# Optimization experiments

Measured on AMD Instinct MI355X. Metric: run time of the kernel, lower is better.

Reference implementation:

```python
import jax, jax.numpy as jnp
import numpy as np

BN_EPS = 1e-5

def setup_inputs() -> dict:
    key = jax.random.key(0)
    ks = jax.random.split(key, 6)
    B, C, H, W, K = 16, 512, 64, 64, 32
    return {
        "x": jax.random.normal(ks[0], (B, C, H, W), dtype=jnp.float32),
        "conv_w": jax.random.normal(ks[1], (C, C), dtype=jnp.float32) * (1.0 / np.sqrt(C)),
        "conv_b": jax.random.normal(ks[2], (C,), dtype=jnp.float32) * 0.01,
        "codewords": jax.random.normal(ks[3], (K, C), dtype=jnp.float32) * (1.0 / np.sqrt(C)),
        "scale": jax.random.uniform(ks[4], (K,), dtype=jnp.float32, minval=-1.0, maxval=0.0),
        "bn_gamma": jnp.ones((K,), jnp.float32),
        "bn_beta": jnp.zeros((K,), jnp.float32),
        "bn_mean": jnp.zeros((K,), jnp.float32),
        "bn_var": jnp.ones((K,), jnp.float32),
        "fc_w": jax.random.normal(ks[5], (C, C), dtype=jnp.float32) * (1.0 / np.sqrt(C)),
        "fc_b": jnp.zeros((C,), jnp.float32),
    }

def reference(x, conv_w, conv_b, codewords, scale, bn_gamma, bn_beta, bn_mean, bn_var, fc_w, fc_b):
    B, C, H, W = x.shape
    N = H * W
    # 1x1 conv projection: (B,C,H,W) x (O,C) -> (B,O,H,W)
    proj = jnp.einsum('bchw,oc->bohw', x, conv_w) + conv_b[None, :, None, None]
    z = proj.reshape(B, C, N).transpose(0, 2, 1)  # (B, N, C)
    # scaled L2 distances without materializing (B,N,K,C):
    # ||z - cw||^2 = ||z||^2 - 2 z.cw + ||cw||^2
    z_sq = jnp.sum(z * z, axis=-1)                     # (B, N)
    cw_sq = jnp.sum(codewords * codewords, axis=-1)    # (K,)
    cross = jnp.einsum('bnc,kc->bnk', z, codewords)    # (B, N, K)
    dist = scale[None, None, :] * (z_sq[:, :, None] - 2.0 * cross + cw_sq[None, None, :])
    assign = jax.nn.softmax(dist, axis=2)              # (B, N, K)
    # aggregate: sum_n a[b,n,k] * (z[b,n,c] - cw[k,c])
    enc = jnp.einsum('bnk,bnc->bkc', assign, z) - jnp.sum(assign, axis=1)[:, :, None] * codewords[None]  # (B, K, C)
    # BatchNorm1d(num_codes) in eval mode normalizes the K (feature) axis, then ReLU
    inv_std = jax.lax.rsqrt(bn_var + BN_EPS)
    enc_bn = (enc - bn_mean[None, :, None]) * (inv_std * bn_gamma)[None, :, None] + bn_beta[None, :, None]
    encoding_feat = jnp.mean(jax.nn.relu(enc_bn), axis=1)  # (B, C)
    # sigmoid channel gate + residual fuse
    gamma = jax.nn.sigmoid(encoding_feat @ fc_w.T + fc_b)  # (B, C)
    y = gamma[:, :, None, None]
    output = jax.nn.relu(x + x * y)
    return (encoding_feat, output)
```

## Files before the change

kernel.cpp:

```cpp
#include <hip/hip_runtime.h>
#include <hip/hip_bf16.h>
#include <stdint.h>

#define DEV static __device__ __forceinline__

typedef __attribute__((ext_vector_type(8))) short bf16x8;
typedef __attribute__((ext_vector_type(4))) float f32x4;

DEV void async_ld16(const void* g, void* l) {
  __builtin_amdgcn_global_load_lds(
      (const __attribute__((address_space(1))) void*)g,
      (__attribute__((address_space(3))) void*)l, 16, 0, 0);
}

DEV unsigned short f2bf(float f) {
  union { __hip_bfloat16 h; unsigned short u; } c;
  c.h = __float2bfloat16(f);
  return c.u;
}

#define Bb 16
#define Cc 512
#define Nn 4096
#define Kk 32
#define NSPLIT 32

__global__ void k_castw(const float* __restrict__ a, __hip_bfloat16* __restrict__ o) {
  int i = blockIdx.x * 256 + threadIdx.x;
  o[i] = __float2bfloat16(a[i]);
}

__global__ void k_cw(const float* __restrict__ cw, __hip_bfloat16* __restrict__ cwb,
                     float* __restrict__ cwsq) {
  int k = blockIdx.x, lane = threadIdx.x;
  float s = 0.f;
#pragma unroll
  for (int j = 0; j < 8; ++j) {
    float v = cw[k * Cc + lane * 8 + j];
    cwb[k * Cc + lane * 8 + j] = __float2bfloat16(v);
    s += v * v;
  }
  for (int off = 32; off; off >>= 1) s += __shfl_down(s, off);
  if (lane == 0) cwsq[k] = s;
}

__global__ __launch_bounds__(256, 4) void k_gemm_z(const float* __restrict__ X,
                                                   const __hip_bfloat16* __restrict__ Bw,
                                                   const float* __restrict__ bias,
                                                   __hip_bfloat16* __restrict__ Z) {
  constexpr int AE = 128 * 32;
  constexpr int BE = 128 * 32;
  __shared__ __align__(16) unsigned short As[2 * AE];
  __shared__ __align__(16) __hip_bfloat16 Bs[2 * BE];
  const int b = blockIdx.y;
  const int n0 = (blockIdx.x & 31) * 128;
  const int c0 = (blockIdx.x >> 5) * 128;
  const int tid = threadIdx.x;
  const int lane = tid & 63, wid = tid >> 6;
  const int wr = (wid >> 1) * 64, wc = (wid & 1) * 64;
  const int cg = tid & 7;
  const int ng = tid >> 3;
  const float* Xb = X + (size_t)b * Cc * Nn + n0 + ng * 4;
  const __hip_bfloat16* Bbp = Bw + (size_t)c0 * Cc;
  f32x4 acc[4][4] = {};
  float4 av[4];
#pragma unroll
  for (int i = 0; i < 4; ++i)
    av[i] = *(const float4*)&Xb[(size_t)(cg * 4 + i) * Nn];
  int cur = 0;
  for (int kt = 0; kt < 16; ++kt) {
    unsigned short* Aw = As + cur * AE;
#pragma unroll
    for (int j = 0; j < 4; ++j) {
      int row = ng * 4 + j;
      int q = (cg >> 1) ^ ((row >> 1) & 3);
      ushort4 w;
      w.x = f2bf(av[0][j]);
      w.y = f2bf(av[1][j]);
      w.z = f2bf(av[2][j]);
      w.w = f2bf(av[3][j]);
      *(ushort4*)&Aw[row * 32 + q * 8 + (cg & 1) * 4] = w;
    }
    char* Bwr = (char*)(Bs + cur * BE);
#pragma unroll
    for (int j = 0; j < 2; ++j) {
      int li = tid + j * 256;
      int row = li >> 2;
      int kc = ((li & 3) ^ ((li >> 3) & 3)) * 8;
      async_ld16(Bbp + (size_t)row * Cc + kt * 32 + kc, Bwr + li * 16);
    }
    __syncthreads();
    if (kt < 15) {
#pragma unroll
      for (int i = 0; i < 4; ++i)
        av[i] = *(const float4*)&Xb[(size_t)((kt + 1) * 32 + cg * 4 + i) * Nn];
    }
    const unsigned short* Ar = As + cur * AE;
    const __hip_bfloat16* Br = Bs + cur * BE;
    bf16x8 af[4], bfv[4];
#pragma unroll
    for (int m = 0; m < 4; ++m) {
      int row = wr + m * 16 + (lane & 15);
      int q = (lane >> 4) ^ ((row >> 1) & 3);
      af[m] = *(const bf16x8*)&Ar[row * 32 + q * 8];
    }
#pragma unroll
    for (int nf = 0; nf < 4; ++nf) {
      int row = wc + nf * 16 + (lane & 15);
      int q = (lane >> 4) ^ ((row >> 1) & 3);
      bfv[nf] = *(const bf16x8*)&Br[row * 32 + q * 8];
    }
#pragma unroll
    for (int m = 0; m < 4; ++m)
#pragma unroll
      for (int nf = 0; nf < 4; ++nf)
        acc[m][nf] = __builtin_amdgcn_mfma_f32_16x16x32_bf16(af[m], bfv[nf], acc[m][nf], 0, 0, 0);
    cur ^= 1;
  }
  __hip_bfloat16* Zb = Z + ((size_t)b * Nn + n0) * Cc + c0;
#pragma unroll
  for (int nf = 0; nf < 4; ++nf) {
    int col = wc + nf * 16 + (lane & 15);
    float bv = bias[c0 + col];
#pragma unroll
    for (int m = 0; m < 4; ++m) {
#pragma unroll
      for (int r = 0; r < 4; ++r) {
        int row = wr + m * 16 + (lane >> 4) * 4 + r;
        Zb[(size_t)row * Cc + col] = __float2bfloat16(acc[m][nf][r] + bv);
      }
    }
  }
}

__global__ __launch_bounds__(256) void k_cross(const __hip_bfloat16* __restrict__ Z,
                                               const __hip_bfloat16* __restrict__ CW,
                                               const float* __restrict__ scale,
                                               const float* __restrict__ cwsq,
                                               float* __restrict__ assign,
                                               float* __restrict__ asum) {
  __shared__ __align__(16) __hip_bfloat16 As[128 * 32];
  __shared__ __align__(16) __hip_bfloat16 Bs[32 * 32];
  __shared__ float s_zsq[128];
  __shared__ float s_asum[Kk];
  int b = blockIdx.y;
  int n0 = blockIdx.x * 128;
  int tid = threadIdx.x, lane = tid & 63, wid = tid >> 6;
  if (tid < Kk) s_asum[tid] = 0.f;
  const __hip_bfloat16* Ab = Z + ((size_t)b * Nn + n0) * Cc;
  f32x4 acc[2][2] = {};
  float sq = 0.f;
  for (int kt = 0; kt < 16; ++kt) {
    int k0 = kt * 32;
    __syncthreads();
#pragma unroll
    for (int j = 0; j < 2; ++j) {
      int li = tid + j * 256;
      int row = li >> 2;
      int kc = ((li & 3) ^ ((li >> 3) & 3)) * 8;
      async_ld16(Ab + (size_t)row * Cc + k0 + kc, (char*)As + li * 16);
    }
    if (tid < 128) {
      int row = tid >> 2;
      int kc = ((tid & 3) ^ ((tid >> 3) & 3)) * 8;
      async_ld16(CW + (size_t)row * Cc + k0 + kc, (char*)Bs + tid * 16);
    }
    __syncthreads();
    {
      int row = tid >> 1, h = tid & 1;
      int rsw = (row >> 1) & 3;
#pragma unroll
      for (int c8 = 0; c8 < 2; ++c8) {
        union { bf16x8 v; __hip_bfloat16 e[8]; } t;
        t.v = *(const bf16x8*)&As[row * 32 + (((2 * h + c8) ^ rsw) * 8)];
#pragma unroll
        for (int i = 0; i < 8; ++i) {
          float v = __bfloat162float(t.e[i]);
          sq += v * v;
        }
      }
    }
    bf16x8 af[2], bfv[2];
#pragma unroll
    for (int m = 0; m < 2; ++m) {
      int row = wid * 32 + m * 16 + (lane & 15);
      int q = (lane >> 4) ^ ((row >> 1) & 3);
      af[m] = *(const bf16x8*)&As[row * 32 + q * 8];
    }
#pragma unroll
    for (int nf = 0; nf < 2; ++nf) {
      int row = nf * 16 + (lane & 15);
      int q = (lane >> 4) ^ ((row >> 1) & 3);
      bfv[nf] = *(const bf16x8*)&Bs[row * 32 + q * 8];
    }
#pragma unroll
    for (int m = 0; m < 2; ++m)
#pragma unroll
      for (int nf = 0; nf < 2; ++nf)
        acc[m][nf] = __builtin_amdgcn_mfma_f32_16x16x32_bf16(af[m], bfv[nf], acc[m][nf], 0, 0, 0);
  }
  sq += __shfl_xor(sq, 1);
  if ((tid & 1) == 0) s_zsq[tid >> 1] = sq;
  __syncthreads();
  float sc[2], cq[2];
#pragma unroll
  for (int nf = 0; nf < 2; ++nf) {
    sc[nf] = scale[nf * 16 + (lane & 15)];
    cq[nf] = cwsq[nf * 16 + (lane & 15)];
  }
  float asump0 = 0.f, asump1 = 0.f;
#pragma unroll
  for (int m = 0; m < 2; ++m) {
#pragma unroll
    for (int r = 0; r < 4; ++r) {
      int row = wid * 32 + m * 16 + (lane >> 4) * 4 + r;
      float zq = s_zsq[row];
      float v0 = sc[0] * (zq - 2.f * acc[m][0][r] + cq[0]);
      float v1 = sc[1] * (zq - 2.f * acc[m][1][r] + cq[1]);
      float mx = fmaxf(v0, v1);
#pragma unroll
      for (int off = 1; off < 16; off <<= 1) mx = fmaxf(mx, __shfl_xor(mx, off));
      float e0 = __expf(v0 - mx), e1 = __expf(v1 - mx);
      float s = e0 + e1;
#pragma unroll
      for (int off = 1; off < 16; off <<= 1) s += __shfl_xor(s, off);
      float inv = 1.f / s;
      float a0 = e0 * inv, a1 = e1 * inv;
      acc[m][0][r] = a0;
      acc[m][1][r] = a1;
      asump0 += a0;
      asump1 += a1;
    }
  }
  asump0 += __shfl_xor(asump0, 16); asump0 += __shfl_xor(asump0, 32);
  asump1 += __shfl_xor(asump1, 16); asump1 += __shfl_xor(asump1, 32);
  if (lane < 16) {
    atomicAdd(&s_asum[lane], asump0);
    atomicAdd(&s_asum[16 + lane], asump1);
  }
  float* Cb = assign + ((size_t)b * Nn + n0) * Kk;
#pragma unroll
  for (int m = 0; m < 2; ++m)
#pragma unroll
    for (int nf = 0; nf < 2; ++nf) {
      int col = nf * 16 + (lane & 15);
#pragma unroll
      for (int r = 0; r < 4; ++r) {
        int row = wid * 32 + m * 16 + (lane >> 4) * 4 + r;
        Cb[(size_t)row * Kk + col] = acc[m][nf][r];
      }
    }
  __syncthreads();
  if (tid < Kk) atomicAdd(&asum[b * Kk + tid], s_asum[tid]);
}

__global__ __launch_bounds__(256) void k_enc_part(const float* __restrict__ assign,
                                                  const __hip_bfloat16* __restrict__ Z,
                                                  float* __restrict__ part) {
  __shared__ float sa[128][Kk];
  int b = blockIdx.z;
  int s = blockIdx.y;
  int c = blockIdx.x * 256 + threadIdx.x;
  int tid = threadIdx.x;
  int n0 = s * 128;
  const float* ap = assign + ((size_t)b * Nn + n0) * Kk;
  for (int i = tid; i < 128 * Kk; i += 256) sa[i >> 5][i & 31] = ap[i];
  __syncthreads();
  float acc[Kk];
#pragma unroll
  for (int k = 0; k < Kk; ++k) acc[k] = 0.f;
  const __hip_bfloat16* zp = Z + ((size_t)b * Nn + n0) * Cc + c;
  for (int n = 0; n < 128; ++n) {
    float zv = __bfloat162float(zp[(size_t)n * Cc]);
    const float4* sp = (const float4*)&sa[n][0];
#pragma unroll
    for (int q = 0; q < 8; ++q) {
      float4 a4 = sp[q];
      acc[4 * q + 0] = fmaf(a4.x, zv, acc[4 * q + 0]);
      acc[4 * q + 1] = fmaf(a4.y, zv, acc[4 * q + 1]);
      acc[4 * q + 2] = fmaf(a4.z, zv, acc[4 * q + 2]);
      acc[4 * q + 3] = fmaf(a4.w, zv, acc[4 * q + 3]);
    }
  }
  float* pp = part + (((size_t)s * Bb + b) * Kk) * Cc + c;
#pragma unroll
  for (int k = 0; k < Kk; ++k) pp[(size_t)k * Cc] = acc[k];
}

__global__ __launch_bounds__(256) void k_enc_bn(const float* __restrict__ part,
                                                const float* __restrict__ asum,
                                                const float* __restrict__ cw,
                                                const float* __restrict__ bn_g,
                                                const float* __restrict__ bn_b,
                                                const float* __restrict__ bn_m,
                                                const float* __restrict__ bn_v,
                                                float* __restrict__ ef) {
  int bk = blockIdx.x;
  int b = bk >> 5, k = bk & 31;
  int tid = threadIdx.x;
  float g = bn_g[k], bt = bn_b[k], mn = bn_m[k], iv = rsqrtf(bn_v[k] + 1e-5f);
  float as = asum[bk];
  for (int c = tid; c < Cc; c += 256) {
    float e = 0.f;
#pragma unroll
    for (int s = 0; s < NSPLIT; ++s)
      e += part[(((size_t)s * Bb + b) * Kk + k) * Cc + c];
    e -= as * cw[k * Cc + c];
    e = (e - mn) * (iv * g) + bt;
    e = fmaxf(e, 0.f);
    atomicAdd(&ef[b * Cc + c], e * (1.f / 32.f));
  }
}

__global__ void k_fc(const float* __restrict__ ef, const float* __restrict__ fcw,
                     const float* __restrict__ fcb, float* __restrict__ gamma) {
  int b = blockIdx.x;
  int o = blockIdx.y * 4 + (threadIdx.x >> 6);
  int lane = threadIdx.x & 63;
  const float* w = fcw + (size_t)o * Cc;
  const float* e = ef + b * Cc;
  float s = 0.f;
#pragma unroll
  for (int j = 0; j < 8; ++j) s += e[lane + j * 64] * w[lane + j * 64];
  for (int off = 32; off; off >>= 1) s += __shfl_down(s, off);
  if (lane == 0) gamma[b * Cc + o] = 1.f / (1.f + __expf(-(s + fcb[o])));
}

__global__ __launch_bounds__(256) void k_out(const float* __restrict__ x,
                                             const float* __restrict__ gamma,
                                             float* __restrict__ out) {
  int bc = blockIdx.x;
  float m = 1.f + gamma[bc];
  size_t base = (size_t)bc * (Nn / 4);
  const float4* xp = (const float4*)x + base;
  float4* op = (float4*)out + base;
#pragma unroll
  for (int j = 0; j < 4; ++j) {
    int i = j * 256 + threadIdx.x;
    float4 v = xp[i];
    float4 r;
    r.x = fmaxf(v.x * m, 0.f);
    r.y = fmaxf(v.y * m, 0.f);
    r.z = fmaxf(v.z * m, 0.f);
    r.w = fmaxf(v.w * m, 0.f);
    op[i] = r;
  }
}

extern "C" void kernel_launch(void* const* d_in, const int* in_sizes, int n_in,
                              void* d_out, int out_size, void* d_ws, size_t ws_size,
                              hipStream_t stream) {
  const float* x = (const float*)d_in[0];
  const float* conv_w = (const float*)d_in[1];
  const float* conv_b = (const float*)d_in[2];
  const float* codewords = (const float*)d_in[3];
  const float* scale = (const float*)d_in[4];
  const float* bn_gamma = (const float*)d_in[5];
  const float* bn_beta = (const float*)d_in[6];
  const float* bn_mean = (const float*)d_in[7];
  const float* bn_var = (const float*)d_in[8];
  const float* fc_w = (const float*)d_in[9];
  const float* fc_b = (const float*)d_in[10];

  float* ef_out = (float*)d_out;
  float* out = (float*)d_out + Bb * Cc;

  char* ws = (char*)d_ws;
  size_t off = 0;
  float* part = (float*)(ws + off);
  off += (size_t)NSPLIT * Bb * Kk * Cc * 4;
  __hip_bfloat16* z = (__hip_bfloat16*)(ws + off);
  off += (size_t)Bb * Nn * Cc * 2;
  float* assign = (float*)(ws + off);
  off += (size_t)Bb * Nn * Kk * 4;
  __hip_bfloat16* wbf = (__hip_bfloat16*)(ws + off);
  off += (size_t)Cc * Cc * 2;
  __hip_bfloat16* cwb = (__hip_bfloat16*)(ws + off);
  off += (size_t)Kk * Cc * 2;
  float* cwsq = (float*)(ws + off);
  off += 512;
  float* asum = (float*)(ws + off);
  off += (size_t)Bb * Kk * 4;
  float* gamma = (float*)(ws + off);
  off += (size_t)Bb * Cc * 4;
  (void)ws_size; (void)n_in; (void)in_sizes; (void)out_size;

  hipMemsetAsync(asum, 0, Bb * Kk * 4, stream);
  hipMemsetAsync(ef_out, 0, Bb * Cc * 4, stream);

  k_castw<<<dim3(Cc * Cc / 256), dim3(256), 0, stream>>>(conv_w, wbf);
  k_cw<<<dim3(Kk), dim3(64), 0, stream>>>(codewords, cwb, cwsq);
  k_gemm_z<<<dim3((Nn / 128) * 4, Bb), dim3(256), 0, stream>>>(x, wbf, conv_b, z);
  k_cross<<<dim3(Nn / 128, Bb), dim3(256), 0, stream>>>(z, cwb, scale, cwsq, assign, asum);
  k_enc_part<<<dim3(Cc / 256, NSPLIT, Bb), dim3(256), 0, stream>>>(assign, z, part);
  k_enc_bn<<<dim3(Bb * Kk), dim3(256), 0, stream>>>(part, asum, codewords, bn_gamma, bn_beta,
                                                    bn_mean, bn_var, ef_out);
  k_fc<<<dim3(Bb, Cc / 4), dim3(256), 0, stream>>>(ef_out, fc_w, fc_b, gamma);
  k_out<<<dim3(Bb * Cc), dim3(256), 0, stream>>>(x, gamma, out);
}
```

Before: 206.1 us.

## Widen z GEMM tile to 256 channels with warp-specialized A/B loaders

The 1x1-conv GEMM now uses 512-thread blocks covering 128 positions by 256 output channels, which halves the number of times x is read and converted per batch. Half the threads convert fp32 x into a padded, XOR-swizzled LDS tile, while the other half prefetch the next weight tile into the alternate buffer with async LDS loads. The larger tile increases LDS use and register pressure and cuts the grid size, so occupancy may drop. The A-fragment read is split into two 8-byte loads because of the new padded layout.

```diff
diff --git a/kernel.cpp b/kernel.cpp
--- a/kernel.cpp
+++ b/kernel.cpp
@@ -44,56 +44,74 @@
   if (lane == 0) cwsq[k] = s;
 }
 
-__global__ __launch_bounds__(256, 4) void k_gemm_z(const float* __restrict__ X,
-                                                   const __hip_bfloat16* __restrict__ Bw,
-                                                   const float* __restrict__ bias,
-                                                   __hip_bfloat16* __restrict__ Z) {
-  constexpr int AE = 128 * 32;
-  constexpr int BE = 128 * 32;
+__global__ __launch_bounds__(512) void k_gemm_z(const float* __restrict__ X,
+                                                const __hip_bfloat16* __restrict__ Bw,
+                                                const float* __restrict__ bias,
+                                                __hip_bfloat16* __restrict__ Z) {
+  constexpr int LDA = 36;
+  constexpr int AE = 128 * LDA;
+  constexpr int BE = 256 * 32;
   __shared__ __align__(16) unsigned short As[2 * AE];
   __shared__ __align__(16) __hip_bfloat16 Bs[2 * BE];
   const int b = blockIdx.y;
   const int n0 = (blockIdx.x & 31) * 128;
-  const int c0 = (blockIdx.x >> 5) * 128;
+  const int c0 = (blockIdx.x >> 5) * 256;
   const int tid = threadIdx.x;
   const int lane = tid & 63, wid = tid >> 6;
-  const int wr = (wid >> 1) * 64, wc = (wid & 1) * 64;
-  const int cg = tid & 7;
-  const int ng = tid >> 3;
+  const int wr = (wid >> 2) * 64, wc = (wid & 3) * 64;
+  const bool aHalf = tid < 256;
+  const int cg = (tid & 255) >> 5;
+  const int ng = tid & 31;
+  const int tb = tid & 255;
   const float* Xb = X + (size_t)b * Cc * Nn + n0 + ng * 4;
   const __hip_bfloat16* Bbp = Bw + (size_t)c0 * Cc;
   f32x4 acc[4][4] = {};
   float4 av[4];
-#pragma unroll
-  for (int i = 0; i < 4; ++i)
-    av[i] = *(const float4*)&Xb[(size_t)(cg * 4 + i) * Nn];
+  if (aHalf) {
+#pragma unroll
+    for (int i = 0; i < 4; ++i)
+      av[i] = *(const float4*)&Xb[(size_t)(cg * 4 + i) * Nn];
+  } else {
+#pragma unroll
+    for (int j = 0; j < 4; ++j) {
+      int li = tb + j * 256;
+      int row = li >> 2;
+      int kc = ((li & 3) ^ ((li >> 3) & 3)) * 8;
+      async_ld16(Bbp + (size_t)row * Cc + kc, (char*)Bs + li * 16);
+    }
+  }
   int cur = 0;
   for (int kt = 0; kt < 16; ++kt) {
-    unsigned short* Aw = As + cur * AE;
-#pragma unroll
-    for (int j = 0; j < 4; ++j) {
-      int row = ng * 4 + j;
-      int q = (cg >> 1) ^ ((row >> 1) & 3);
-      ushort4 w;
-      w.x = f2bf(av[0][j]);
-      w.y = f2bf(av[1][j]);
-      w.z = f2bf(av[2][j]);
-      w.w = f2bf(av[3][j]);
-      *(ushort4*)&Aw[row * 32 + q * 8 + (cg & 1) * 4] = w;
-    }
-    char* Bwr = (char*)(Bs + cur * BE);
-#pragma unroll
-    for (int j = 0; j < 2; ++j) {
-      int li = tid + j * 256;
-      int row = li >> 2;
-      int kc = ((li & 3) ^ ((li >> 3) & 3)) * 8;
-      async_ld16(Bbp + (size_t)row * Cc + kt * 32 + kc, Bwr + li * 16);
+    if (aHalf) {
+      unsigned short* Aw = As + cur * AE;
+#pragma unroll
+      for (int j = 0; j < 4; ++j) {
+        int n = ng * 4 + j;
+        int slot = cg ^ (ng & 7);
+        ushort4 w;
+        w.x = f2bf(av[0][j]);
+        w.y = f2bf(av[1][j]);
+        w.z = f2bf(av[2][j]);
+        w.w = f2bf(av[3][j]);
+        *(ushort4*)&Aw[n * LDA + slot * 4] = w;
+      }
     }
     __syncthreads();
     if (kt < 15) {
-#pragma unroll
-      for (int i = 0; i < 4; ++i)
-        av[i] = *(const float4*)&Xb[(size_t)((kt + 1) * 32 + cg * 4 + i) * Nn];
+      if (aHalf) {
+#pragma unroll
+        for (int i = 0; i < 4; ++i)
+          av[i] = *(const float4*)&Xb[(size_t)((kt + 1) * 32 + cg * 4 + i) * Nn];
+      } else {
+        char* Bwr = (char*)(Bs + (cur ^ 1) * BE);
+#pragma unroll
+        for (int j = 0; j < 4; ++j) {
+          int li = tb + j * 256;
+          int row = li >> 2;
+          int kc = ((li & 3) ^ ((li >> 3) & 3)) * 8;
+          async_ld16(Bbp + (size_t)row * Cc + (kt + 1) * 32 + kc, Bwr + li * 16);
+        }
+      }
     }
     const unsigned short* Ar = As + cur * AE;
     const __hip_bfloat16* Br = Bs + cur * BE;
@@ -101,8 +119,13 @@
 #pragma unroll
     for (int m = 0; m < 4; ++m) {
       int row = wr + m * 16 + (lane & 15);
-      int q = (lane >> 4) ^ ((row >> 1) & 3);
-      af[m] = *(const bf16x8*)&Ar[row * 32 + q * 8];
+      int h = (row >> 2) & 7;
+      int g = lane >> 4;
+      int s0 = (2 * g) ^ h, s1 = (2 * g + 1) ^ h;
+      union { ushort4 u2[2]; bf16x8 v8; } t;
+      t.u2[0] = *(const ushort4*)&Ar[row * LDA + s0 * 4];
+      t.u2[1] = *(const ushort4*)&Ar[row * LDA + s1 * 4];
+      af[m] = t.v8;
     }
 #pragma unroll
     for (int nf = 0; nf < 4; ++nf) {
@@ -390,7 +413,7 @@
 
   k_castw<<<dim3(Cc * Cc / 256), dim3(256), 0, stream>>>(conv_w, wbf);
   k_cw<<<dim3(Kk), dim3(64), 0, stream>>>(codewords, cwb, cwsq);
-  k_gemm_z<<<dim3((Nn / 128) * 4, Bb), dim3(256), 0, stream>>>(x, wbf, conv_b, z);
+  k_gemm_z<<<dim3((Nn / 128) * 2, Bb), dim3(512), 0, stream>>>(x, wbf, conv_b, z);
   k_cross<<<dim3(Nn / 128, Bb), dim3(256), 0, stream>>>(z, cwb, scale, cwsq, assign, asum);
   k_enc_part<<<dim3(Cc / 256, NSPLIT, Bb), dim3(256), 0, stream>>>(assign, z, part);
   k_enc_bn<<<dim3(Bb * Kk), dim3(256), 0, stream>>>(part, asum, codewords, bn_gamma, bn_beta,
```

Result: no change. 204.4 us (-0.8%).

## Deepen k_gemm_z prefetch to two stages and re-layout A tile in LDS

Applied to the files above, without the earlier changes.

Restructures the projection GEMM main loop. X fp32 loads are now prefetched two k-steps ahead in two register buffers, and the async B loads are issued for the next stage right after the barrier. The A tile in LDS gets a padded stride (36) with a new XOR slot swizzle and a different thread mapping (cg = tid>>5, ng = tid&31), and is read back as two 8-byte halves. The goal is to hide global load latency and cut LDS bank conflicts on the A writes. In exchange it uses more registers (the occupancy hint of 4 was dropped) and more LDS.

```diff
diff --git a/kernel.cpp b/kernel.cpp
--- a/kernel.cpp
+++ b/kernel.cpp
@@ -44,11 +44,12 @@
   if (lane == 0) cwsq[k] = s;
 }
 
-__global__ __launch_bounds__(256, 4) void k_gemm_z(const float* __restrict__ X,
-                                                   const __hip_bfloat16* __restrict__ Bw,
-                                                   const float* __restrict__ bias,
-                                                   __hip_bfloat16* __restrict__ Z) {
-  constexpr int AE = 128 * 32;
+__global__ __launch_bounds__(256) void k_gemm_z(const float* __restrict__ X,
+                                                const __hip_bfloat16* __restrict__ Bw,
+                                                const float* __restrict__ bias,
+                                                __hip_bfloat16* __restrict__ Z) {
+  constexpr int LDA = 36;
+  constexpr int AE = 128 * LDA;
   constexpr int BE = 128 * 32;
   __shared__ __align__(16) unsigned short As[2 * AE];
   __shared__ __align__(16) __hip_bfloat16 Bs[2 * BE];
@@ -58,65 +59,95 @@
   const int tid = threadIdx.x;
   const int lane = tid & 63, wid = tid >> 6;
   const int wr = (wid >> 1) * 64, wc = (wid & 1) * 64;
-  const int cg = tid & 7;
-  const int ng = tid >> 3;
+  const int cg = tid >> 5;
+  const int ng = tid & 31;
+  const int slot = cg ^ (ng & 7);
   const float* Xb = X + (size_t)b * Cc * Nn + n0 + ng * 4;
   const __hip_bfloat16* Bbp = Bw + (size_t)c0 * Cc;
   f32x4 acc[4][4] = {};
-  float4 av[4];
+  float4 av0[4], av1[4];
 #pragma unroll
   for (int i = 0; i < 4; ++i)
-    av[i] = *(const float4*)&Xb[(size_t)(cg * 4 + i) * Nn];
+    av0[i] = *(const float4*)&Xb[(size_t)(cg * 4 + i) * Nn];
+#pragma unroll
+  for (int i = 0; i < 4; ++i)
+    av1[i] = *(const float4*)&Xb[(size_t)(32 + cg * 4 + i) * Nn];
+#pragma unroll
+  for (int j = 0; j < 2; ++j) {
+    int li = tid + j * 256;
+    int row = li >> 2;
+    int kc = ((li & 3) ^ ((li >> 3) & 3)) * 8;
+    async_ld16(Bbp + (size_t)row * Cc + kc, (char*)Bs + li * 16);
+  }
   int cur = 0;
-  for (int kt = 0; kt < 16; ++kt) {
-    unsigned short* Aw = As + cur * AE;
-#pragma unroll
-    for (int j = 0; j < 4; ++j) {
-      int row = ng * 4 + j;
-      int q = (cg >> 1) ^ ((row >> 1) & 3);
-      ushort4 w;
-      w.x = f2bf(av[0][j]);
-      w.y = f2bf(av[1][j]);
-      w.z = f2bf(av[2][j]);
-      w.w = f2bf(av[3][j]);
-      *(ushort4*)&Aw[row * 32 + q * 8 + (cg & 1) * 4] = w;
-    }
-    char* Bwr = (char*)(Bs + cur * BE);
-#pragma unroll
-    for (int j = 0; j < 2; ++j) {
-      int li = tid + j * 256;
-      int row = li >> 2;
-      int kc = ((li & 3) ^ ((li >> 3) & 3)) * 8;
-      async_ld16(Bbp + (size_t)row * Cc + kt * 32 + kc, Bwr + li * 16);
-    }
-    __syncthreads();
-    if (kt < 15) {
-#pragma unroll
-      for (int i = 0; i < 4; ++i)
-        av[i] = *(const float4*)&Xb[(size_t)((kt + 1) * 32 + cg * 4 + i) * Nn];
-    }
-    const unsigned short* Ar = As + cur * AE;
-    const __hip_bfloat16* Br = Bs + cur * BE;
-    bf16x8 af[4], bfv[4];
-#pragma unroll
-    for (int m = 0; m < 4; ++m) {
-      int row = wr + m * 16 + (lane & 15);
-      int q = (lane >> 4) ^ ((row >> 1) & 3);
-      af[m] = *(const bf16x8*)&Ar[row * 32 + q * 8];
-    }
-#pragma unroll
-    for (int nf = 0; nf < 4; ++nf) {
-      int row = wc + nf * 16 + (lane & 15);
-      int q = (lane >> 4) ^ ((row >> 1) & 3);
-      bfv[nf] = *(const bf16x8*)&Br[row * 32 + q * 8];
-    }
-#pragma unroll
-    for (int m = 0; m < 4; ++m)
-#pragma unroll
-      for (int nf = 0; nf < 4; ++nf)
-        acc[m][nf] = __builtin_amdgcn_mfma_f32_16x16x32_bf16(af[m], bfv[nf], acc[m][nf], 0, 0, 0);
-    cur ^= 1;
-  }
+
+#define GEMM_STEP(KT, AV)                                                      \
+  {                                                                            \
+    unsigned short* Aw = As + cur * AE;                                        \
+    _Pragma("unroll")                                                          \
+    for (int j = 0; j < 4; ++j) {                                              \
+      int n = ng * 4 + j;                                                      \
+      ushort4 w;                                                               \
+      w.x = f2bf(AV[0][j]);                                                    \
+      w.y = f2bf(AV[1][j]);                                                    \
+      w.z = f2bf(AV[2][j]);                                                    \
+      w.w = f2bf(AV[3][j]);                                                    \
+      *(ushort4*)&Aw[n * LDA + slot * 4] = w;                                  \
+    }                                                                          \
+    __syncthreads();                                                           \
+    if ((KT) < 15) {                                                           \
+      char* Bwr = (char*)(Bs + (cur ^ 1) * BE);                                \
+      _Pragma("unroll")                                                        \
+      for (int j = 0; j < 2; ++j) {                                            \
+        int li = tid + j * 256;                                                \
+        int row = li >> 2;                                                     \
+        int kc = ((li & 3) ^ ((li >> 3) & 3)) * 8;                             \
+        async_ld16(Bbp + (size_t)row * Cc + ((KT) + 1) * 32 + kc,              \
+                   Bwr + li * 16);                                             \
+      }                                                                        \
+    }                                                                          \
+    if ((KT) < 14) {                                                           \
+      _Pragma("unroll")                                                        \
+      for (int i = 0; i < 4; ++i)                                              \
+        AV[i] = *(const float4*)&Xb[(size_t)(((KT) + 2) * 32 + cg * 4 + i) *   \
+                                    Nn];                                       \
+    }                                                                          \
+    const unsigned short* Ar = As + cur * AE;                                  \
+    const __hip_bfloat16* Br = Bs + cur * BE;                                  \
+    bf16x8 af[4], bfv[4];                                                      \
+    _Pragma("unroll")                                                          \
+    for (int m = 0; m < 4; ++m) {                                              \
+      int row = wr + m * 16 + (lane & 15);                                     \
+      int h = (row >> 2) & 7;                                                  \
+      int g = lane >> 4;                                                       \
+      int s0 = (2 * g) ^ h, s1 = (2 * g + 1) ^ h;                              \
+      union { ushort4 u2[2]; bf16x8 v8; } t;                                   \
+      t.u2[0] = *(const ushort4*)&Ar[row * LDA + s0 * 4];                      \
+      t.u2[1] = *(const ushort4*)&Ar[row * LDA + s1 * 4];                      \
+      af[m] = t.v8;                                                            \
+    }                                                                          \
+    _Pragma("unroll")                                                          \
+    for (int nf = 0; nf < 4; ++nf) {                                           \
+      int row = wc + nf * 16 + (lane & 15);                                    \
+      int q = (lane >> 4) ^ ((row >> 1) & 3);                                  \
+      bfv[nf] = *(const bf16x8*)&Br[row * 32 + q * 8];                         \
+    }                                                                          \
+    _Pragma("unroll")                                                          \
+    for (int m = 0; m < 4; ++m)                                                \
+      _Pragma("unroll")                                                        \
+      for (int nf = 0; nf < 4; ++nf)                                           \
+        acc[m][nf] =                                                           \
+            __builtin_amdgcn_mfma_f32_16x16x32_bf16(af[m], bfv[nf],            \
+                                                    acc[m][nf], 0, 0, 0);      \
+    cur ^= 1;                                                                  \
+  }
+
+  for (int kt = 0; kt < 16; kt += 2) {
+    GEMM_STEP(kt, av0)
+    GEMM_STEP(kt + 1, av1)
+  }
+#undef GEMM_STEP
+
   __hip_bfloat16* Zb = Z + ((size_t)b * Nn + n0) * Cc + c0;
 #pragma unroll
   for (int nf = 0; nf < 4; ++nf) {
```

Result: faster. 190.8 us (-7.4%).
